# Kernel tuning notes

Hardware: AMD Instinct MI355X
Metric: run time of the kernel (lower is better)

The kernel has to match this reference:

```python
import jax, jax.numpy as jnp
import numpy as np

B, N, NEMBED, E, H = 4, 256, 10000, 63, 128
D = E + 1  # feature dim after concat = 64


def _lin(key, fan_in, fan_out):
    k1, k2 = jax.random.split(key)
    bound = 1.0 / np.sqrt(fan_in)
    W = jax.random.uniform(k1, (fan_in, fan_out), jnp.float32, -bound, bound)
    b = jax.random.uniform(k2, (fan_out,), jnp.float32, -bound, bound)
    return W, b


def setup_inputs() -> dict:
    key = jax.random.key(0)
    ks = jax.random.split(key, 9)
    xcat = jax.random.randint(ks[0], (B, N), 0, NEMBED, dtype=jnp.int64)
    xfeat = jax.random.normal(ks[1], (B, N), dtype=jnp.float32)
    emb = jax.random.normal(ks[2], (NEMBED, E), dtype=jnp.float32)
    W1, b1 = _lin(ks[3], D, H)
    W2, b2 = _lin(ks[4], H, H)
    W3, b3 = _lin(ks[5], H, H)
    D1, c1 = _lin(ks[6], H, H)
    D2, c2 = _lin(ks[7], H, H)
    D3, c3 = _lin(ks[8], H, 1)
    return {"xcat": xcat, "xfeat": xfeat, "emb": emb,
            "W1": W1, "b1": b1, "W2": W2, "b2": b2, "W3": W3, "b3": b3,
            "D1": D1, "c1": c1, "D2": D2, "c2": c2, "D3": D3, "c3": c3}


def reference(xcat, xfeat, emb, W1, b1, W2, b2, W3, b3, D1, c1, D2, c2, D3, c3):
    # embed + concat scalar feature -> [B, N, D]
    x = jnp.concatenate([emb[xcat], xfeat[..., None]], axis=-1)
    # pairwise outer product over the set dim -> [B, N, N, D]
    # (original: einsum 'bid,bjd->bdij' then permute(0,2,3,1) == 'bid,bjd->bijd')
    p = jnp.einsum('bid,bjd->bijd', x, x)
    # per-pair 3-layer MLP (enc)
    h = jnp.maximum(p @ W1 + b1, 0.0)
    h = jnp.maximum(h @ W2 + b2, 0.0)
    h = h @ W3 + b3
    # relu -> mean pool over (i, j) -> relu; dropout is identity in eval
    h = jnp.maximum(h, 0.0)
    h = jnp.mean(h, axis=(1, 2))  # [B, H]
    h = jnp.maximum(h, 0.0)
    # dec MLP -> [B, 1]
    h = jnp.maximum(h @ D1 + c1, 0.0)
    h = jnp.maximum(h @ D2 + c2, 0.0)
    return h @ D3 + c3
```

## Files before the change

kernel.cpp:

```cpp
#include <hip/hip_runtime.h>
#include <hip/hip_bf16.h>


#define NB 4
#define NN 256
#define HD 128

typedef __attribute__((ext_vector_type(8))) short bf16x8;
typedef __attribute__((ext_vector_type(4))) short short4v;
typedef __attribute__((ext_vector_type(4))) float f32x4;

__device__ __forceinline__ short f2bf(float f) {
    unsigned u = __builtin_bit_cast(unsigned, f);
    u = (u + 0x7fff + ((u >> 16) & 1)) >> 16;
    return (short)u;
}

__device__ __forceinline__ void tri_ij(int t, int& i, int& j) {
    j = (int)((sqrtf(8.0f * (float)t + 1.0f) - 1.0f) * 0.5f);
    while (((j + 1) * (j + 2) >> 1) <= t) ++j;
    while (((j * (j + 1)) >> 1) > t) --j;
    i = t - ((j * (j + 1)) >> 1);
}

__device__ __forceinline__ void pack_w(const float* __restrict__ W, short* __restrict__ pw,
                                       int KQ, int u) {
    int l  = u & 63;
    int kq = (u >> 6) % KQ;
    int mt = (u >> 6) / KQ;
    int q = l >> 4, m = l & 15;
    int c = mt * 16 + m;
#pragma unroll
    for (int j = 0; j < 8; ++j) {
        int k = kq * 32 + q * 8 + j;
        pw[u * 8 + j] = f2bf(W[k * 128 + c]);
    }
}

__global__ void prep_kernel(const int* __restrict__ xcat,
                            const float* __restrict__ xfeat,
                            const float* __restrict__ emb,
                            const float* __restrict__ W1,
                            const float* __restrict__ W2,
                            const float* __restrict__ W3,
                            float* __restrict__ x,
                            short* __restrict__ pw1,
                            short* __restrict__ pw2,
                            short* __restrict__ pw3)
{
    int bid = blockIdx.x;
    int tid = threadIdx.x;
    if (bid < 256) {
        int f = bid * 256 + tid;
        int d = f & 63;
        int nn = f >> 6;
        float v;
        if (d < 63) v = emb[xcat[nn] * 63 + d];
        else        v = xfeat[nn];
        x[f] = v;
    } else if (bid < 260) {
        pack_w(W1, pw1, 2, (bid - 256) * 256 + tid);
    } else if (bid < 268) {
        pack_w(W2, pw2, 4, (bid - 260) * 256 + tid);
    } else {
        pack_w(W3, pw3, 4, (bid - 268) * 256 + tid);
    }
}

__global__ __launch_bounds__(256, 3) void pair_mlp(
    const float* __restrict__ x,
    const short* __restrict__ pw1, const float* __restrict__ b1,
    const short* __restrict__ pw2, const float* __restrict__ b2,
    const short* __restrict__ pw3, const float* __restrict__ b3,
    float* __restrict__ partialOut)
{
    __shared__ short smP[128 * 64];
    __shared__ short smH[128 * 128];
    __shared__ float smW[128];

    const int tid = threadIdx.x;
    const int l = tid & 63;
    const int w = __builtin_amdgcn_readfirstlane(tid >> 6);
    const int wm = w >> 1;
    const int wn = w & 1;
    const int q = l >> 4;
    const int m = l & 15;
    const int b = blockIdx.y;
    const int tbase = blockIdx.x * 128;
    const float* xb = x + (b << 14);
    char* smPc = (char*)smP;
    char* smHc = (char*)smH;

    {
        const int p = tid >> 1;
        const int half = tid & 1;
        int i, j;
        tri_ij(tbase + p, i, j);
        if (half == 0) smW[p] = (i == j) ? 1.0f : 2.0f;
        const float4* xi4 = (const float4*)(xb + (i << 6) + half * 32);
        const float4* xj4 = (const float4*)(xb + (j << 6) + half * 32);
#pragma unroll
        for (int c = 0; c < 4; ++c) {
            float4 a0 = xi4[2 * c], a1 = xi4[2 * c + 1];
            float4 u0 = xj4[2 * c], u1 = xj4[2 * c + 1];
            bf16x8 s;
            s[0] = f2bf(a0.x * u0.x); s[1] = f2bf(a0.y * u0.y);
            s[2] = f2bf(a0.z * u0.z); s[3] = f2bf(a0.w * u0.w);
            s[4] = f2bf(a1.x * u1.x); s[5] = f2bf(a1.y * u1.y);
            s[6] = f2bf(a1.z * u1.z); s[7] = f2bf(a1.w * u1.w);
            int chunk = half * 4 + c;
            int phys = chunk ^ (p & 7);
            *(bf16x8*)(smPc + p * 128 + phys * 16) = s;
        }
    }
    __syncthreads();

    f32x4 acc[4][4];
    const f32x4 zero = {0.f, 0.f, 0.f, 0.f};

#pragma unroll
    for (int mt = 0; mt < 4; ++mt)
#pragma unroll
        for (int nt = 0; nt < 4; ++nt) acc[mt][nt] = zero;

#pragma unroll
    for (int kq = 0; kq < 2; ++kq) {
        bf16x8 bfr[4], afr[4];
#pragma unroll
        for (int nt = 0; nt < 4; ++nt) {
            int pair = wn * 64 + nt * 16 + m;
            int phys = (kq * 4 + q) ^ (pair & 7);
            bfr[nt] = *(const bf16x8*)(smPc + pair * 128 + phys * 16);
        }
#pragma unroll
        for (int mt = 0; mt < 4; ++mt)
            afr[mt] = *(const bf16x8*)(pw1 + ((((wm * 4 + mt) * 2 + kq) * 64 + l) << 3));
#pragma unroll
        for (int mt = 0; mt < 4; ++mt)
#pragma unroll
            for (int nt = 0; nt < 4; ++nt)
                acc[mt][nt] = __builtin_amdgcn_mfma_f32_16x16x32_bf16(afr[mt], bfr[nt], acc[mt][nt], 0, 0, 0);
    }

#pragma unroll
    for (int mt = 0; mt < 4; ++mt) {
        int mtg = wm * 4 + mt;
        float4 bv = *(const float4*)(b1 + mtg * 16 + q * 4);
#pragma unroll
        for (int nt = 0; nt < 4; ++nt) {
            int pair = wn * 64 + nt * 16 + m;
            short4v sv;
            sv[0] = f2bf(fmaxf(acc[mt][nt][0] + bv.x, 0.f));
            sv[1] = f2bf(fmaxf(acc[mt][nt][1] + bv.y, 0.f));
            sv[2] = f2bf(fmaxf(acc[mt][nt][2] + bv.z, 0.f));
            sv[3] = f2bf(fmaxf(acc[mt][nt][3] + bv.w, 0.f));
            int chunk = mtg * 2 + (q >> 1);
            int phys = chunk ^ (pair & 15);
            *(short4v*)(smHc + pair * 256 + phys * 16 + (q & 1) * 8) = sv;
        }
    }
    __syncthreads();

#pragma unroll
    for (int mt = 0; mt < 4; ++mt)
#pragma unroll
        for (int nt = 0; nt < 4; ++nt) acc[mt][nt] = zero;

#pragma unroll
    for (int kq = 0; kq < 4; ++kq) {
        bf16x8 bfr[4], afr[4];
#pragma unroll
        for (int nt = 0; nt < 4; ++nt) {
            int pair = wn * 64 + nt * 16 + m;
            int phys = (kq * 4 + q) ^ (pair & 15);
            bfr[nt] = *(const bf16x8*)(smHc + pair * 256 + phys * 16);
        }
#pragma unroll
        for (int mt = 0; mt < 4; ++mt)
            afr[mt] = *(const bf16x8*)(pw2 + ((((wm * 4 + mt) * 4 + kq) * 64 + l) << 3));
#pragma unroll
        for (int mt = 0; mt < 4; ++mt)
#pragma unroll
            for (int nt = 0; nt < 4; ++nt)
                acc[mt][nt] = __builtin_amdgcn_mfma_f32_16x16x32_bf16(afr[mt], bfr[nt], acc[mt][nt], 0, 0, 0);
    }
    __syncthreads();

#pragma unroll
    for (int mt = 0; mt < 4; ++mt) {
        int mtg = wm * 4 + mt;
        float4 bv = *(const float4*)(b2 + mtg * 16 + q * 4);
#pragma unroll
        for (int nt = 0; nt < 4; ++nt) {
            int pair = wn * 64 + nt * 16 + m;
            short4v sv;
            sv[0] = f2bf(fmaxf(acc[mt][nt][0] + bv.x, 0.f));
            sv[1] = f2bf(fmaxf(acc[mt][nt][1] + bv.y, 0.f));
            sv[2] = f2bf(fmaxf(acc[mt][nt][2] + bv.z, 0.f));
            sv[3] = f2bf(fmaxf(acc[mt][nt][3] + bv.w, 0.f));
            int chunk = mtg * 2 + (q >> 1);
            int phys = chunk ^ (pair & 15);
            *(short4v*)(smHc + pair * 256 + phys * 16 + (q & 1) * 8) = sv;
        }
    }
    __syncthreads();

#pragma unroll
    for (int mt = 0; mt < 4; ++mt)
#pragma unroll
        for (int nt = 0; nt < 4; ++nt) acc[mt][nt] = zero;

#pragma unroll
    for (int kq = 0; kq < 4; ++kq) {
        bf16x8 bfr[4], afr[4];
#pragma unroll
        for (int nt = 0; nt < 4; ++nt) {
            int pair = wn * 64 + nt * 16 + m;
            int phys = (kq * 4 + q) ^ (pair & 15);
            bfr[nt] = *(const bf16x8*)(smHc + pair * 256 + phys * 16);
        }
#pragma unroll
        for (int mt = 0; mt < 4; ++mt)
            afr[mt] = *(const bf16x8*)(pw3 + ((((wm * 4 + mt) * 4 + kq) * 64 + l) << 3));
#pragma unroll
        for (int mt = 0; mt < 4; ++mt)
#pragma unroll
            for (int nt = 0; nt < 4; ++nt)
                acc[mt][nt] = __builtin_amdgcn_mfma_f32_16x16x32_bf16(afr[mt], bfr[nt], acc[mt][nt], 0, 0, 0);
    }

    float wpv[4];
#pragma unroll
    for (int nt = 0; nt < 4; ++nt)
        wpv[nt] = smW[wn * 64 + nt * 16 + m];

    float* smPart = (float*)smP;
#pragma unroll
    for (int mt = 0; mt < 4; ++mt) {
        int mtg = wm * 4 + mt;
        float4 bv = *(const float4*)(b3 + mtg * 16 + q * 4);
        float vs0 = 0.f, vs1 = 0.f, vs2 = 0.f, vs3 = 0.f;
#pragma unroll
        for (int nt = 0; nt < 4; ++nt) {
            vs0 += wpv[nt] * fmaxf(acc[mt][nt][0] + bv.x, 0.f);
            vs1 += wpv[nt] * fmaxf(acc[mt][nt][1] + bv.y, 0.f);
            vs2 += wpv[nt] * fmaxf(acc[mt][nt][2] + bv.z, 0.f);
            vs3 += wpv[nt] * fmaxf(acc[mt][nt][3] + bv.w, 0.f);
        }
#pragma unroll
        for (int s = 1; s < 16; s <<= 1) {
            vs0 += __shfl_xor(vs0, s, 64);
            vs1 += __shfl_xor(vs1, s, 64);
            vs2 += __shfl_xor(vs2, s, 64);
            vs3 += __shfl_xor(vs3, s, 64);
        }
        if (m == 0) {
            float* p = smPart + wn * HD + mtg * 16 + q * 4;
            p[0] = vs0; p[1] = vs1; p[2] = vs2; p[3] = vs3;
        }
    }
    __syncthreads();

    if (tid < HD) {
        float v = smPart[tid] + smPart[HD + tid];
        partialOut[(b * 257 + blockIdx.x) * HD + tid] = v;
    }
}

__global__ __launch_bounds__(128) void reduce1(const float* __restrict__ partial,
                                               float* __restrict__ partial2)
{
    const int ch = threadIdx.x;
    const int g = blockIdx.x;
    const int b = blockIdx.y;
    const float* base = partial + (b * 257 + g * 16) * HD + ch;
    float s = 0.f;
#pragma unroll
    for (int t = 0; t < 16; ++t) {
        int tl = g * 16 + t;
        s += (tl < 257) ? base[t * HD] : 0.f;
    }
    partial2[(b * 17 + g) * HD + ch] = s;
}

__global__ void reduce_decode(const float* __restrict__ partial2,
                              const float* __restrict__ D1, const float* __restrict__ c1,
                              const float* __restrict__ D2, const float* __restrict__ c2,
                              const float* __restrict__ D3, const float* __restrict__ c3,
                              float* __restrict__ out)
{
    __shared__ float red[2][HD];
    __shared__ float hb[HD];
    __shared__ float tb[HD];
    const int b = blockIdx.x;
    const int t = threadIdx.x;
    const int ch = t & 127, hf = t >> 7;

    float s = 0.f;
#pragma unroll
    for (int g = 0; g < 9; ++g) {
        int tl = hf * 9 + g;
        s += (tl < 17) ? partial2[(b * 17 + tl) * HD + ch] : 0.f;
    }
    red[hf][ch] = s;
    __syncthreads();
    if (hf == 0)
        hb[ch] = fmaxf((red[0][ch] + red[1][ch]) * (1.0f / 65536.0f), 0.0f);
    __syncthreads();

    float a = 0.f;
    for (int k = hf * 64; k < hf * 64 + 64; ++k)
        a = fmaf(hb[k], D1[(k << 7) + ch], a);
    red[hf][ch] = a;
    __syncthreads();
    if (hf == 0)
        tb[ch] = fmaxf(red[0][ch] + red[1][ch] + c1[ch], 0.0f);
    __syncthreads();

    a = 0.f;
    for (int k = hf * 64; k < hf * 64 + 64; ++k)
        a = fmaf(tb[k], D2[(k << 7) + ch], a);
    red[hf][ch] = a;
    __syncthreads();
    if (hf == 0)
        hb[ch] = fmaxf(red[0][ch] + red[1][ch] + c2[ch], 0.0f);
    __syncthreads();

    if (hf == 0) red[0][ch] = hb[ch] * D3[ch];
    __syncthreads();
    if (t < 64) {
        float r = red[0][t] + red[0][t + 64];
#pragma unroll
        for (int s2 = 1; s2 < 64; s2 <<= 1)
            r += __shfl_xor(r, s2, 64);
        if (t == 0) out[b] = r + c3[0];
    }
}

extern "C" void kernel_launch(void* const* d_in, const int* in_sizes, int n_in,
                              void* d_out, int out_size, void* d_ws, size_t ws_size,
                              hipStream_t stream)
{
    (void)in_sizes; (void)n_in; (void)out_size; (void)ws_size;

    const int*   xcat  = (const int*)  d_in[0];
    const float* xfeat = (const float*)d_in[1];
    const float* emb   = (const float*)d_in[2];
    const float* W1    = (const float*)d_in[3];
    const float* b1    = (const float*)d_in[4];
    const float* W2    = (const float*)d_in[5];
    const float* b2    = (const float*)d_in[6];
    const float* W3    = (const float*)d_in[7];
    const float* b3    = (const float*)d_in[8];
    const float* D1    = (const float*)d_in[9];
    const float* c1    = (const float*)d_in[10];
    const float* D2    = (const float*)d_in[11];
    const float* c2    = (const float*)d_in[12];
    const float* D3    = (const float*)d_in[13];
    const float* c3    = (const float*)d_in[14];
    float* out = (float*)d_out;

    float* x        = (float*)d_ws;
    short* pw1      = (short*)(x + NB * NN * 64);
    short* pw2      = pw1 + 8 * 2 * 64 * 8;
    short* pw3      = pw2 + 8 * 4 * 64 * 8;
    float* partial  = (float*)(pw3 + 8 * 4 * 64 * 8);
    float* partial2 = partial + NB * 257 * HD;

    prep_kernel<<<276, 256, 0, stream>>>(xcat, xfeat, emb, W1, W2, W3,
                                         x, pw1, pw2, pw3);
    pair_mlp<<<dim3(257, NB), 256, 0, stream>>>(x, pw1, b1, pw2, b2, pw3, b3, partial);
    reduce1<<<dim3(17, NB), 128, 0, stream>>>(partial, partial2);
    reduce_decode<<<NB, 256, 0, stream>>>(partial2, D1, c1, D2, c2, D3, c3, out);
}
```

Before: 129.5 us.

## Halve pair tile per block to 64 pairs, raising occupancy and block count

Shrinks each pair_mlp block from 128 to 64 pairs, which halves LDS use and the accumulator registers per wave. Launch bounds go from 3 to 6 blocks per SM and the grid doubles to 514 blocks per batch. Biases are now loaded as the initial MFMA accumulator values instead of being added afterwards, and bf16 conversion packs two values per op. The trade-off is that every block reloads the weight fragments for half as much work, and reduce1 now sums 32 partials per group instead of 16.

```diff
diff --git a/kernel.cpp b/kernel.cpp
--- a/kernel.cpp
+++ b/kernel.cpp
@@ -5,10 +5,18 @@
 #define NB 4
 #define NN 256
 #define HD 128
+#define TPB 514
 
 typedef __attribute__((ext_vector_type(8))) short bf16x8;
-typedef __attribute__((ext_vector_type(4))) short short4v;
 typedef __attribute__((ext_vector_type(4))) float f32x4;
+
+__device__ __forceinline__ unsigned rne2(float a, float b) {
+    unsigned ua = __builtin_bit_cast(unsigned, a);
+    unsigned ub = __builtin_bit_cast(unsigned, b);
+    ua = ua + 0x7fff + ((ua >> 16) & 1);
+    ub = ub + 0x7fff + ((ub >> 16) & 1);
+    return (ua >> 16) | (ub & 0xffff0000u);
+}
 
 __device__ __forceinline__ short f2bf(float f) {
     unsigned u = __builtin_bit_cast(unsigned, f);
@@ -67,16 +75,16 @@
     }
 }
 
-__global__ __launch_bounds__(256, 3) void pair_mlp(
+__global__ __launch_bounds__(256, 6) void pair_mlp(
     const float* __restrict__ x,
     const short* __restrict__ pw1, const float* __restrict__ b1,
     const short* __restrict__ pw2, const float* __restrict__ b2,
     const short* __restrict__ pw3, const float* __restrict__ b3,
     float* __restrict__ partialOut)
 {
-    __shared__ short smP[128 * 64];
-    __shared__ short smH[128 * 128];
-    __shared__ float smW[128];
+    __shared__ short smP[64 * 64];
+    __shared__ short smH[64 * 128];
+    __shared__ float smW[64];
 
     const int tid = threadIdx.x;
     const int l = tid & 63;
@@ -86,49 +94,50 @@
     const int q = l >> 4;
     const int m = l & 15;
     const int b = blockIdx.y;
-    const int tbase = blockIdx.x * 128;
+    const int tbase = blockIdx.x * 64;
     const float* xb = x + (b << 14);
     char* smPc = (char*)smP;
     char* smHc = (char*)smH;
 
     {
-        const int p = tid >> 1;
-        const int half = tid & 1;
+        const int p = tid >> 2;
+        const int qr = tid & 3;
         int i, j;
         tri_ij(tbase + p, i, j);
-        if (half == 0) smW[p] = (i == j) ? 1.0f : 2.0f;
-        const float4* xi4 = (const float4*)(xb + (i << 6) + half * 32);
-        const float4* xj4 = (const float4*)(xb + (j << 6) + half * 32);
-#pragma unroll
-        for (int c = 0; c < 4; ++c) {
+        if (qr == 0) smW[p] = (i == j) ? 1.0f : 2.0f;
+        const float4* xi4 = (const float4*)(xb + (i << 6) + qr * 16);
+        const float4* xj4 = (const float4*)(xb + (j << 6) + qr * 16);
+#pragma unroll
+        for (int c = 0; c < 2; ++c) {
             float4 a0 = xi4[2 * c], a1 = xi4[2 * c + 1];
             float4 u0 = xj4[2 * c], u1 = xj4[2 * c + 1];
-            bf16x8 s;
-            s[0] = f2bf(a0.x * u0.x); s[1] = f2bf(a0.y * u0.y);
-            s[2] = f2bf(a0.z * u0.z); s[3] = f2bf(a0.w * u0.w);
-            s[4] = f2bf(a1.x * u1.x); s[5] = f2bf(a1.y * u1.y);
-            s[6] = f2bf(a1.z * u1.z); s[7] = f2bf(a1.w * u1.w);
-            int chunk = half * 4 + c;
+            uint4 s;
+            s.x = rne2(a0.x * u0.x, a0.y * u0.y);
+            s.y = rne2(a0.z * u0.z, a0.w * u0.w);
+            s.z = rne2(a1.x * u1.x, a1.y * u1.y);
+            s.w = rne2(a1.z * u1.z, a1.w * u1.w);
+            int chunk = qr * 2 + c;
             int phys = chunk ^ (p & 7);
-            *(bf16x8*)(smPc + p * 128 + phys * 16) = s;
-        }
-    }
-    __syncthreads();
-
-    f32x4 acc[4][4];
-    const f32x4 zero = {0.f, 0.f, 0.f, 0.f};
-
-#pragma unroll
-    for (int mt = 0; mt < 4; ++mt)
-#pragma unroll
-        for (int nt = 0; nt < 4; ++nt) acc[mt][nt] = zero;
+            *(uint4*)(smPc + p * 128 + phys * 16) = s;
+        }
+    }
+    __syncthreads();
+
+    f32x4 acc[4][2];
+
+#pragma unroll
+    for (int mt = 0; mt < 4; ++mt) {
+        float4 bv = *(const float4*)(b1 + (wm * 4 + mt) * 16 + q * 4);
+        f32x4 init = {bv.x, bv.y, bv.z, bv.w};
+        acc[mt][0] = init; acc[mt][1] = init;
+    }
 
 #pragma unroll
     for (int kq = 0; kq < 2; ++kq) {
-        bf16x8 bfr[4], afr[4];
-#pragma unroll
-        for (int nt = 0; nt < 4; ++nt) {
-            int pair = wn * 64 + nt * 16 + m;
+        bf16x8 bfr[2], afr[4];
+#pragma unroll
+        for (int nt = 0; nt < 2; ++nt) {
+            int pair = wn * 32 + nt * 16 + m;
             int phys = (kq * 4 + q) ^ (pair & 7);
             bfr[nt] = *(const bf16x8*)(smPc + pair * 128 + phys * 16);
         }
@@ -138,40 +147,39 @@
 #pragma unroll
         for (int mt = 0; mt < 4; ++mt)
 #pragma unroll
-            for (int nt = 0; nt < 4; ++nt)
+            for (int nt = 0; nt < 2; ++nt)
                 acc[mt][nt] = __builtin_amdgcn_mfma_f32_16x16x32_bf16(afr[mt], bfr[nt], acc[mt][nt], 0, 0, 0);
     }
 
 #pragma unroll
     for (int mt = 0; mt < 4; ++mt) {
         int mtg = wm * 4 + mt;
-        float4 bv = *(const float4*)(b1 + mtg * 16 + q * 4);
-#pragma unroll
-        for (int nt = 0; nt < 4; ++nt) {
-            int pair = wn * 64 + nt * 16 + m;
-            short4v sv;
-            sv[0] = f2bf(fmaxf(acc[mt][nt][0] + bv.x, 0.f));
-            sv[1] = f2bf(fmaxf(acc[mt][nt][1] + bv.y, 0.f));
-            sv[2] = f2bf(fmaxf(acc[mt][nt][2] + bv.z, 0.f));
-            sv[3] = f2bf(fmaxf(acc[mt][nt][3] + bv.w, 0.f));
+#pragma unroll
+        for (int nt = 0; nt < 2; ++nt) {
+            int pair = wn * 32 + nt * 16 + m;
+            uint2 sv;
+            sv.x = rne2(fmaxf(acc[mt][nt][0], 0.f), fmaxf(acc[mt][nt][1], 0.f));
+            sv.y = rne2(fmaxf(acc[mt][nt][2], 0.f), fmaxf(acc[mt][nt][3], 0.f));
             int chunk = mtg * 2 + (q >> 1);
             int phys = chunk ^ (pair & 15);
-            *(short4v*)(smHc + pair * 256 + phys * 16 + (q & 1) * 8) = sv;
-        }
-    }
-    __syncthreads();
-
-#pragma unroll
-    for (int mt = 0; mt < 4; ++mt)
-#pragma unroll
-        for (int nt = 0; nt < 4; ++nt) acc[mt][nt] = zero;
+            *(uint2*)(smHc + pair * 256 + phys * 16 + (q & 1) * 8) = sv;
+        }
+    }
+    __syncthreads();
+
+#pragma unroll
+    for (int mt = 0; mt < 4; ++mt) {
+        float4 bv = *(const float4*)(b2 + (wm * 4 + mt) * 16 + q * 4);
+        f32x4 init = {bv.x, bv.y, bv.z, bv.w};
+        acc[mt][0] = init; acc[mt][1] = init;
+    }
 
 #pragma unroll
     for (int kq = 0; kq < 4; ++kq) {
-        bf16x8 bfr[4], afr[4];
-#pragma unroll
-        for (int nt = 0; nt < 4; ++nt) {
-            int pair = wn * 64 + nt * 16 + m;
+        bf16x8 bfr[2], afr[4];
+#pragma unroll
+        for (int nt = 0; nt < 2; ++nt) {
+            int pair = wn * 32 + nt * 16 + m;
             int phys = (kq * 4 + q) ^ (pair & 15);
             bfr[nt] = *(const bf16x8*)(smHc + pair * 256 + phys * 16);
         }
@@ -181,7 +189,7 @@
 #pragma unroll
         for (int mt = 0; mt < 4; ++mt)
 #pragma unroll
-            for (int nt = 0; nt < 4; ++nt)
+            for (int nt = 0; nt < 2; ++nt)
                 acc[mt][nt] = __builtin_amdgcn_mfma_f32_16x16x32_bf16(afr[mt], bfr[nt], acc[mt][nt], 0, 0, 0);
     }
     __syncthreads();
@@ -189,33 +197,32 @@
 #pragma unroll
     for (int mt = 0; mt < 4; ++mt) {
         int mtg = wm * 4 + mt;
-        float4 bv = *(const float4*)(b2 + mtg * 16 + q * 4);
-#pragma unroll
-        for (int nt = 0; nt < 4; ++nt) {
-            int pair = wn * 64 + nt * 16 + m;
-            short4v sv;
-            sv[0] = f2bf(fmaxf(acc[mt][nt][0] + bv.x, 0.f));
-            sv[1] = f2bf(fmaxf(acc[mt][nt][1] + bv.y, 0.f));
-            sv[2] = f2bf(fmaxf(acc[mt][nt][2] + bv.z, 0.f));
-            sv[3] = f2bf(fmaxf(acc[mt][nt][3] + bv.w, 0.f));
+#pragma unroll
+        for (int nt = 0; nt < 2; ++nt) {
+            int pair = wn * 32 + nt * 16 + m;
+            uint2 sv;
+            sv.x = rne2(fmaxf(acc[mt][nt][0], 0.f), fmaxf(acc[mt][nt][1], 0.f));
+            sv.y = rne2(fmaxf(acc[mt][nt][2], 0.f), fmaxf(acc[mt][nt][3], 0.f));
             int chunk = mtg * 2 + (q >> 1);
             int phys = chunk ^ (pair & 15);
-            *(short4v*)(smHc + pair * 256 + phys * 16 + (q & 1) * 8) = sv;
-        }
-    }
-    __syncthreads();
-
-#pragma unroll
-    for (int mt = 0; mt < 4; ++mt)
-#pragma unroll
-        for (int nt = 0; nt < 4; ++nt) acc[mt][nt] = zero;
+            *(uint2*)(smHc + pair * 256 + phys * 16 + (q & 1) * 8) = sv;
+        }
+    }
+    __syncthreads();
+
+#pragma unroll
+    for (int mt = 0; mt < 4; ++mt) {
+        float4 bv = *(const float4*)(b3 + (wm * 4 + mt) * 16 + q * 4);
+        f32x4 init = {bv.x, bv.y, bv.z, bv.w};
+        acc[mt][0] = init; acc[mt][1] = init;
+    }
 
 #pragma unroll
     for (int kq = 0; kq < 4; ++kq) {
-        bf16x8 bfr[4], afr[4];
-#pragma unroll
-        for (int nt = 0; nt < 4; ++nt) {
-            int pair = wn * 64 + nt * 16 + m;
+        bf16x8 bfr[2], afr[4];
+#pragma unroll
+        for (int nt = 0; nt < 2; ++nt) {
+            int pair = wn * 32 + nt * 16 + m;
             int phys = (kq * 4 + q) ^ (pair & 15);
             bfr[nt] = *(const bf16x8*)(smHc + pair * 256 + phys * 16);
         }
@@ -225,45 +232,35 @@
 #pragma unroll
         for (int mt = 0; mt < 4; ++mt)
 #pragma unroll
-            for (int nt = 0; nt < 4; ++nt)
+            for (int nt = 0; nt < 2; ++nt)
                 acc[mt][nt] = __builtin_amdgcn_mfma_f32_16x16x32_bf16(afr[mt], bfr[nt], acc[mt][nt], 0, 0, 0);
     }
 
-    float wpv[4];
-#pragma unroll
-    for (int nt = 0; nt < 4; ++nt)
-        wpv[nt] = smW[wn * 64 + nt * 16 + m];
+    float wpv0 = smW[wn * 32 + m];
+    float wpv1 = smW[wn * 32 + 16 + m];
 
     float* smPart = (float*)smP;
 #pragma unroll
     for (int mt = 0; mt < 4; ++mt) {
         int mtg = wm * 4 + mt;
-        float4 bv = *(const float4*)(b3 + mtg * 16 + q * 4);
-        float vs0 = 0.f, vs1 = 0.f, vs2 = 0.f, vs3 = 0.f;
-#pragma unroll
-        for (int nt = 0; nt < 4; ++nt) {
-            vs0 += wpv[nt] * fmaxf(acc[mt][nt][0] + bv.x, 0.f);
-            vs1 += wpv[nt] * fmaxf(acc[mt][nt][1] + bv.y, 0.f);
-            vs2 += wpv[nt] * fmaxf(acc[mt][nt][2] + bv.z, 0.f);
-            vs3 += wpv[nt] * fmaxf(acc[mt][nt][3] + bv.w, 0.f);
-        }
-#pragma unroll
-        for (int s = 1; s < 16; s <<= 1) {
-            vs0 += __shfl_xor(vs0, s, 64);
-            vs1 += __shfl_xor(vs1, s, 64);
-            vs2 += __shfl_xor(vs2, s, 64);
-            vs3 += __shfl_xor(vs3, s, 64);
+        float vs[4];
+#pragma unroll
+        for (int r = 0; r < 4; ++r) {
+            vs[r] = wpv0 * fmaxf(acc[mt][0][r], 0.f) + wpv1 * fmaxf(acc[mt][1][r], 0.f);
+#pragma unroll
+            for (int s = 1; s < 16; s <<= 1)
+                vs[r] += __shfl_xor(vs[r], s, 64);
         }
         if (m == 0) {
             float* p = smPart + wn * HD + mtg * 16 + q * 4;
-            p[0] = vs0; p[1] = vs1; p[2] = vs2; p[3] = vs3;
+            p[0] = vs[0]; p[1] = vs[1]; p[2] = vs[2]; p[3] = vs[3];
         }
     }
     __syncthreads();
 
     if (tid < HD) {
         float v = smPart[tid] + smPart[HD + tid];
-        partialOut[(b * 257 + blockIdx.x) * HD + tid] = v;
+        partialOut[(b * TPB + blockIdx.x) * HD + tid] = v;
     }
 }
 
@@ -273,12 +270,12 @@
     const int ch = threadIdx.x;
     const int g = blockIdx.x;
     const int b = blockIdx.y;
-    const float* base = partial + (b * 257 + g * 16) * HD + ch;
+    const float* base = partial + (b * TPB + g * 32) * HD + ch;
     float s = 0.f;
 #pragma unroll
-    for (int t = 0; t < 16; ++t) {
-        int tl = g * 16 + t;
-        s += (tl < 257) ? base[t * HD] : 0.f;
+    for (int t = 0; t < 32; ++t) {
+        int tl = g * 32 + t;
+        s += (tl < TPB) ? base[t * HD] : 0.f;
     }
     partial2[(b * 17 + g) * HD + ch] = s;
 }
@@ -365,11 +362,11 @@
     short* pw2      = pw1 + 8 * 2 * 64 * 8;
     short* pw3      = pw2 + 8 * 4 * 64 * 8;
     float* partial  = (float*)(pw3 + 8 * 4 * 64 * 8);
-    float* partial2 = partial + NB * 257 * HD;
+    float* partial2 = partial + NB * TPB * HD;
 
     prep_kernel<<<276, 256, 0, stream>>>(xcat, xfeat, emb, W1, W2, W3,
                                          x, pw1, pw2, pw3);
-    pair_mlp<<<dim3(257, NB), 256, 0, stream>>>(x, pw1, b1, pw2, b2, pw3, b3, partial);
+    pair_mlp<<<dim3(TPB, NB), 256, 0, stream>>>(x, pw1, b1, pw2, b2, pw3, b3, partial);
     reduce1<<<dim3(17, NB), 128, 0, stream>>>(partial, partial2);
     reduce_decode<<<NB, 256, 0, stream>>>(partial2, D1, c1, D2, c2, D3, c3, out);
 }
```

After: 134.6 us. 1.04x slower.
